# Optimization experiments

Measured on AMD Instinct MI355X. Metric: run time of the kernel, lower is better.

## Reference

```python
import jax, jax.numpy as jnp
import numpy as np

DIM = 1024
HEADS = 16
DIM_HEAD = 64
INNER = HEADS * DIM_HEAD  # 1024
EPS = 1e-5


def setup_inputs() -> dict:
    key = jax.random.key(0)
    ks = jax.random.split(key, 8)
    B, N = 4, 2048
    s = 0.02
    return {
        "query": jax.random.normal(ks[0], (B, N, DIM), jnp.float32),
        "key_": jax.random.normal(ks[1], (B, N, DIM), jnp.float32),
        "value": jax.random.normal(ks[2], (B, N, DIM), jnp.float32),
        "Wq": jax.random.normal(ks[3], (DIM, INNER), jnp.float32) * s,
        "Wk": jax.random.normal(ks[4], (DIM, INNER), jnp.float32) * s,
        "Wv": jax.random.normal(ks[5], (DIM, INNER), jnp.float32) * s,
        "Wo": jax.random.normal(ks[6], (INNER, DIM), jnp.float32) * s,
        "bo": jnp.zeros((DIM,), jnp.float32),
        "gamma": jnp.ones((DIM,), jnp.float32),
        "beta": jnp.zeros((DIM,), jnp.float32),
    }


def reference(query, key_, value, Wq, Wk, Wv, Wo, bo, gamma, beta):
    B, N, _ = query.shape
    scale = DIM_HEAD ** (-0.5)
    # project and split heads: [B, H, N, Dh]
    q = (query @ Wq).reshape(B, N, HEADS, DIM_HEAD).transpose(0, 2, 1, 3)
    k = (key_ @ Wk).reshape(B, N, HEADS, DIM_HEAD).transpose(0, 2, 1, 3)
    v = (value @ Wv).reshape(B, N, HEADS, DIM_HEAD).transpose(0, 2, 1, 3)
    dots = jnp.einsum("bhnd,bhmd->bhnm", q, k) * scale  # [B,H,N,N]
    attn = jax.nn.softmax(dots, axis=-1)
    out = jnp.einsum("bhnm,bhmd->bhnd", attn, v)
    out = out.transpose(0, 2, 1, 3).reshape(B, N, INNER)
    out = out @ Wo + bo  # dropout p=0.0 is identity
    # LayerNorm over last dim
    mu = out.mean(-1, keepdims=True)
    var = ((out - mu) ** 2).mean(-1, keepdims=True)
    normed = (out - mu) * jax.lax.rsqrt(var + EPS) * gamma + beta
    return normed + query
```

## Files before the change

kernel.cpp:

```cpp
#include <hip/hip_runtime.h>
#include <stdint.h>

#define K_DIM 1024
#define B_SZ 4
#define N_SEQ 2048
#define HEADS 16
#define DH 64
#define M_TOT (B_SZ * N_SEQ)

typedef __bf16 bf16x8 __attribute__((ext_vector_type(8)));
typedef __bf16 bf16x4 __attribute__((ext_vector_type(4)));
typedef float f32x4 __attribute__((ext_vector_type(4)));
typedef short s16x4 __attribute__((ext_vector_type(4)));

typedef const uint32_t __attribute__((address_space(1))) gas_u32;
typedef uint32_t __attribute__((address_space(3))) las_u32;

#define CE_SCALE 0.1803368801f

__device__ __forceinline__ uint16_t f2bf(float f) {
  uint32_t u = __float_as_uint(f);
  u += 0x7FFFu + ((u >> 16) & 1u);
  return (uint16_t)(u >> 16);
}

__device__ __forceinline__ void gld_lds16(const uint16_t* g, uint16_t* lds) {
  __builtin_amdgcn_global_load_lds((gas_u32*)g, (las_u32*)lds, 16, 0, 0);
}

#if defined(__has_builtin)
#if __has_builtin(__builtin_amdgcn_mfma_f32_16x16x16bf16_1k)
#define HAVE_MFMA16_BUILTIN 1
#endif
#endif

__device__ __forceinline__ f32x4 mfma16(bf16x4 a, bf16x4 b, f32x4 c) {
#ifdef HAVE_MFMA16_BUILTIN
  return __builtin_amdgcn_mfma_f32_16x16x16bf16_1k(
      __builtin_bit_cast(s16x4, a), __builtin_bit_cast(s16x4, b), c, 0, 0, 0);
#else
  f32x4 d;
  asm("v_mfma_f32_16x16x16_bf16 %0, %1, %2, %3"
      : "=v"(d)
      : "v"(a), "v"(b), "v"(c));
  return d;
#endif
}

__global__ __launch_bounds__(256) void conv_bf16_k(const float* __restrict__ s0,
                                                   const float* __restrict__ s1,
                                                   const float* __restrict__ s2,
                                                   uint16_t* __restrict__ dstbase, int n4) {
  const int z = blockIdx.y;
  const float* src = (z == 0) ? s0 : (z == 1) ? s1 : s2;
  uint16_t* dst = dstbase + (size_t)z * M_TOT * K_DIM;
  int i = blockIdx.x * blockDim.x + threadIdx.x;
  if (i < n4) {
    float4 v = ((const float4*)src)[i];
    ushort4 o;
    o.x = f2bf(v.x); o.y = f2bf(v.y); o.z = f2bf(v.z); o.w = f2bf(v.w);
    ((ushort4*)dst)[i] = o;
  }
}

__global__ __launch_bounds__(256) void transpose_conv(const float* __restrict__ s0,
                                                      const float* __restrict__ s1,
                                                      const float* __restrict__ s2,
                                                      const float* __restrict__ s3,
                                                      uint16_t* __restrict__ dstbase) {
  __shared__ float tile[32][33];
  const int z = blockIdx.z;
  const float* src = (z == 0) ? s0 : (z == 1) ? s1 : (z == 2) ? s2 : s3;
  uint16_t* dst = dstbase + (size_t)z * 1024 * 1024;
  const int tx = threadIdx.x, ty = threadIdx.y;
  const int bx = blockIdx.x * 32, by = blockIdx.y * 32;
#pragma unroll
  for (int i = 0; i < 32; i += 8)
    tile[ty + i][tx] = src[(size_t)(by + ty + i) * 1024 + bx + tx];
  __syncthreads();
#pragma unroll
  for (int i = 0; i < 32; i += 8)
    dst[(size_t)(bx + ty + i) * 1024 + by + tx] = f2bf(tile[tx][ty + i]);
}

template <int MODE>
__global__ __launch_bounds__(256, 2) void gemm_bf16(const uint16_t* __restrict__ A,
                                                    const uint16_t* __restrict__ BT,
                                                    void* __restrict__ Cout,
                                                    const float* __restrict__ bias) {
  __shared__ __align__(16) uint16_t As[128 * 32];
  __shared__ __align__(16) uint16_t Bs[128 * 32];
  const int tid = threadIdx.x;
  const int wave = tid >> 6, lane = tid & 63;
  const int g = lane >> 4, c16 = lane & 15;

  const int bid = blockIdx.x;
  const int xcd = bid & 7;
  const int l = bid >> 3;
  const int z = (MODE == 3) ? (l >> 6) : 0;
  const int r = l & 63;
  const int n0 = (r & 7) * 128;
  const int m0 = (xcd * 8 + (r >> 3)) * 128;

  const int wr = wave >> 1, wc = wave & 1;
  float scale = 1.f;
  if (MODE == 3) {
    A += (size_t)z * M_TOT * K_DIM;
    BT += (size_t)z * 1024 * 1024;
    scale = (z == 0) ? CE_SCALE : 1.f;
  }

  const f32x4 fzero = {0.f, 0.f, 0.f, 0.f};
  f32x4 acc[4][4];
#pragma unroll
  for (int i = 0; i < 4; ++i)
#pragma unroll
    for (int j = 0; j < 4; ++j) acc[i][j] = fzero;

  const int srow = wave * 32 + (lane >> 2);
  const int scol = (lane & 3) * 8;
  const uint16_t* ag0 = A + (size_t)(m0 + srow) * K_DIM + scol;
  const uint16_t* ag1 = A + (size_t)(m0 + srow + 16) * K_DIM + scol;
  const uint16_t* bg0 = BT + (size_t)(n0 + srow) * K_DIM + scol;
  const uint16_t* bg1 = BT + (size_t)(n0 + srow + 16) * K_DIM + scol;
  uint16_t* la0 = &As[(wave * 32) * 32];
  uint16_t* la1 = &As[(wave * 32 + 16) * 32];
  uint16_t* lb0 = &Bs[(wave * 32) * 32];
  uint16_t* lb1 = &Bs[(wave * 32 + 16) * 32];

  for (int kt = 0; kt < K_DIM / 32; ++kt) {
    __syncthreads();
    gld_lds16(ag0 + kt * 32, la0);
    gld_lds16(ag1 + kt * 32, la1);
    gld_lds16(bg0 + kt * 32, lb0);
    gld_lds16(bg1 + kt * 32, lb1);
    __syncthreads();
    bf16x8 avec[4], bvec[4];
#pragma unroll
    for (int i = 0; i < 4; ++i)
      avec[i] = *(const bf16x8*)&As[(wr * 64 + i * 16 + c16) * 32 + g * 8];
#pragma unroll
    for (int j = 0; j < 4; ++j)
      bvec[j] = *(const bf16x8*)&Bs[(wc * 64 + j * 16 + c16) * 32 + g * 8];
#pragma unroll
    for (int i = 0; i < 4; ++i)
#pragma unroll
      for (int j = 0; j < 4; ++j)
        acc[i][j] = __builtin_amdgcn_mfma_f32_16x16x32_bf16(avec[i], bvec[j], acc[i][j], 0, 0, 0);
  }

#pragma unroll
  for (int i = 0; i < 4; ++i) {
#pragma unroll
    for (int j = 0; j < 4; ++j) {
      const int col = n0 + wc * 64 + j * 16 + c16;
      if (MODE == 3 && z == 2) {
        const int h = col >> 6, d = col & 63;
        const int row0 = m0 + wr * 64 + i * 16 + g * 4;
        const int b = row0 >> 11, n = row0 & 2047;
        ushort4 o;
        o.x = f2bf(acc[i][j][0]); o.y = f2bf(acc[i][j][1]);
        o.z = f2bf(acc[i][j][2]); o.w = f2bf(acc[i][j][3]);
        *(ushort4*)&((uint16_t*)Cout)[(size_t)2 * M_TOT * 1024 +
                                      (((size_t)(b * HEADS + h)) * DH + d) * N_SEQ + n] = o;
      } else {
#pragma unroll
        for (int r2 = 0; r2 < 4; ++r2) {
          const int row = m0 + wr * 64 + i * 16 + g * 4 + r2;
          if (MODE == 3) {
            const int b = row >> 11, n = row & 2047;
            const int h = col >> 6, d = col & 63;
            ((uint16_t*)Cout)[(size_t)z * M_TOT * 1024 +
                              (((size_t)(b * HEADS + h)) * N_SEQ + n) * DH + d] =
                f2bf(acc[i][j][r2] * scale);
          } else {
            ((float*)Cout)[(size_t)row * 1024 + col] = acc[i][j][r2] + bias[col];
          }
        }
      }
    }
  }
}

__global__ __launch_bounds__(256, 2) void attention_k(const uint16_t* __restrict__ qm,
                                                      const uint16_t* __restrict__ km,
                                                      const uint16_t* __restrict__ vtm,
                                                      uint16_t* __restrict__ om) {
  __shared__ __align__(16) uint16_t Ks[64 * 64];
  __shared__ __align__(16) uint16_t Vs[64 * 64];
  const int tid = threadIdx.x;
  const int wave = tid >> 6, lane = tid & 63;
  const int g = lane >> 4, c16 = lane & 15;

  const int bid = blockIdx.x;
  const int xcd = bid & 7;
  const int l0 = bid >> 3;
  const int bh = xcd * 8 + (l0 & 7);
  const int qblk = l0 >> 3;
  const int b = bh >> 4, h = bh & 15;
  const int q0 = qblk * 256 + wave * 64;

  const uint16_t* qbase = qm + (size_t)bh * N_SEQ * DH;
  const uint16_t* kbase = km + (size_t)bh * N_SEQ * DH;
  const uint16_t* vbase = vtm + (size_t)bh * DH * N_SEQ;

  bf16x8 qf[4][2];
#pragma unroll
  for (int qc = 0; qc < 4; ++qc) {
    const uint16_t* qp = qbase + (size_t)(q0 + qc * 16 + c16) * DH + g * 8;
    qf[qc][0] = *(const bf16x8*)qp;
    qf[qc][1] = *(const bf16x8*)(qp + 32);
  }

  const f32x4 fz = {0.f, 0.f, 0.f, 0.f};
  f32x4 oacc[4][4];
#pragma unroll
  for (int qc = 0; qc < 4; ++qc)
#pragma unroll
    for (int jt = 0; jt < 4; ++jt) oacc[qc][jt] = fz;
  float l[4] = {0.f, 0.f, 0.f, 0.f};

  const int sw = c16 & 7;

  const int ch = tid & 7;
  const int krow0 = tid >> 3, krow1 = (256 + tid) >> 3;
  const int kdst0 = krow0 * 64 + ((ch ^ (krow0 & 7)) << 3);
  const int kdst1 = krow1 * 64 + ((ch ^ (krow1 & 7)) << 3);

  uint4 kp0, kp1, vp0, vp1;
  kp0 = *(const uint4*)&kbase[(size_t)tid * 8];
  kp1 = *(const uint4*)&kbase[(size_t)(256 + tid) * 8];
  vp0 = *(const uint4*)&vbase[(size_t)krow0 * N_SEQ + ch * 8];
  vp1 = *(const uint4*)&vbase[(size_t)krow1 * N_SEQ + ch * 8];
  *(uint4*)&Ks[kdst0] = kp0;
  *(uint4*)&Ks[kdst1] = kp1;
  *(uint4*)&Vs[kdst0] = vp0;
  *(uint4*)&Vs[kdst1] = vp1;
  __syncthreads();

  for (int t = 0; t < N_SEQ / 64; ++t) {
    if (t < N_SEQ / 64 - 1) {
      const size_t ko = (size_t)(t + 1) * 4096;
      const int vc = (t + 1) * 64;
      kp0 = *(const uint4*)&kbase[ko + (size_t)tid * 8];
      kp1 = *(const uint4*)&kbase[ko + (size_t)(256 + tid) * 8];
      vp0 = *(const uint4*)&vbase[(size_t)krow0 * N_SEQ + vc + ch * 8];
      vp1 = *(const uint4*)&vbase[(size_t)krow1 * N_SEQ + vc + ch * 8];
    }

#pragma unroll
    for (int kt = 0; kt < 4; ++kt) {
      const int krow = kt * 16 + c16;
      bf16x8 kf0 = *(const bf16x8*)&Ks[krow * 64 + ((g ^ sw) << 3)];
      bf16x8 kf1 = *(const bf16x8*)&Ks[krow * 64 + (((4 + g) ^ sw) << 3)];
      bf16x4 pk[4];
#pragma unroll
      for (int qc = 0; qc < 4; ++qc) {
        f32x4 z = fz;
        z = __builtin_amdgcn_mfma_f32_16x16x32_bf16(kf0, qf[qc][0], z, 0, 0, 0);
        z = __builtin_amdgcn_mfma_f32_16x16x32_bf16(kf1, qf[qc][1], z, 0, 0, 0);
        const float p0 = __builtin_amdgcn_exp2f(z[0]);
        const float p1 = __builtin_amdgcn_exp2f(z[1]);
        const float p2 = __builtin_amdgcn_exp2f(z[2]);
        const float p3 = __builtin_amdgcn_exp2f(z[3]);
        l[qc] += (p0 + p1) + (p2 + p3);
        bf16x4 pq;
        pq[0] = (__bf16)p0; pq[1] = (__bf16)p1; pq[2] = (__bf16)p2; pq[3] = (__bf16)p3;
        pk[qc] = pq;
      }
#pragma unroll
      for (int jt = 0; jt < 4; ++jt) {
        bf16x4 vb = *(const bf16x4*)&Vs[(jt * 16 + c16) * 64 +
                                        (((kt * 2 + (g >> 1)) ^ sw) << 3) + (g & 1) * 4];
#pragma unroll
        for (int qc = 0; qc < 4; ++qc) oacc[qc][jt] = mfma16(pk[qc], vb, oacc[qc][jt]);
      }
    }

    if (t < N_SEQ / 64 - 1) {
      __syncthreads();
      *(uint4*)&Ks[kdst0] = kp0;
      *(uint4*)&Ks[kdst1] = kp1;
      *(uint4*)&Vs[kdst0] = vp0;
      *(uint4*)&Vs[kdst1] = vp1;
      __syncthreads();
    }
  }

#pragma unroll
  for (int qc = 0; qc < 4; ++qc) {
    l[qc] += __shfl_xor(l[qc], 16);
    l[qc] += __shfl_xor(l[qc], 32);
  }

#pragma unroll
  for (int qc = 0; qc < 4; ++qc) {
#pragma unroll
    for (int r = 0; r < 4; ++r) {
      const float lr = __shfl(l[qc], g * 4 + r, 16);
      const float inv = 1.f / lr;
      const int row = q0 + qc * 16 + g * 4 + r;
      const size_t base = ((size_t)b * N_SEQ + row) * 1024 + h * 64;
#pragma unroll
      for (int jt = 0; jt < 4; ++jt)
        om[base + jt * 16 + c16] = f2bf(oacc[qc][jt][r] * inv);
    }
  }
}

__global__ __launch_bounds__(256) void ln_res_k(const float* __restrict__ proj,
                                                const float* __restrict__ query,
                                                const float* __restrict__ gamma,
                                                const float* __restrict__ beta,
                                                float* __restrict__ out) {
  const int row = blockIdx.x;
  const int tid = threadIdx.x;
  const size_t base = (size_t)row * 1024 + tid * 4;
  float4 v = *(const float4*)(proj + base);
  float s = v.x + v.y + v.z + v.w;
  float s2 = v.x * v.x + v.y * v.y + v.z * v.z + v.w * v.w;
#pragma unroll
  for (int off = 1; off < 64; off <<= 1) {
    s += __shfl_xor(s, off);
    s2 += __shfl_xor(s2, off);
  }
  __shared__ float red[8];
  const int wave = tid >> 6, lane = tid & 63;
  if (lane == 0) { red[wave] = s; red[4 + wave] = s2; }
  __syncthreads();
  s = red[0] + red[1] + red[2] + red[3];
  s2 = red[4] + red[5] + red[6] + red[7];
  const float mu = s * (1.f / 1024.f);
  const float var = fmaxf(s2 * (1.f / 1024.f) - mu * mu, 0.f);
  const float rstd = rsqrtf(var + 1e-5f);
  float4 gq = *(const float4*)(gamma + tid * 4);
  float4 bq = *(const float4*)(beta + tid * 4);
  float4 qq = *(const float4*)(query + base);
  float4 o;
  o.x = (v.x - mu) * rstd * gq.x + bq.x + qq.x;
  o.y = (v.y - mu) * rstd * gq.y + bq.y + qq.y;
  o.z = (v.z - mu) * rstd * gq.z + bq.z + qq.z;
  o.w = (v.w - mu) * rstd * gq.w + bq.w + qq.w;
  *(float4*)(out + base) = o;
}

extern "C" void kernel_launch(void* const* d_in, const int* in_sizes, int n_in,
                              void* d_out, int out_size, void* d_ws, size_t ws_size,
                              hipStream_t stream) {
  (void)in_sizes; (void)n_in; (void)out_size; (void)ws_size;
  const float* query = (const float*)d_in[0];
  const float* key_ = (const float*)d_in[1];
  const float* value = (const float*)d_in[2];
  const float* Wq = (const float*)d_in[3];
  const float* Wk = (const float*)d_in[4];
  const float* Wv = (const float*)d_in[5];
  const float* Wo = (const float*)d_in[6];
  const float* bo = (const float*)d_in[7];
  const float* gamma = (const float*)d_in[8];
  const float* beta = (const float*)d_in[9];
  float* out = (float*)d_out;

  const size_t NELEM = (size_t)M_TOT * 1024;
  uint16_t* wsp = (uint16_t*)d_ws;
  uint16_t* WqT = wsp;
  uint16_t* WoT = WqT + 3 * 1024 * 1024;
  uint16_t* xq = WqT + 4 * 1024 * 1024;
  uint16_t* qb = xq + 3 * NELEM;
  uint16_t* attnO = xq;
  float* proj = (float*)(xq + NELEM);

  const int n4 = (int)(NELEM / 4);
  conv_bf16_k<<<dim3(8192, 3), 256, 0, stream>>>(query, key_, value, xq, n4);

  transpose_conv<<<dim3(32, 32, 4), dim3(32, 8), 0, stream>>>(Wq, Wk, Wv, Wo, WqT);

  gemm_bf16<3><<<1536, 256, 0, stream>>>(xq, WqT, qb, nullptr);

  attention_k<<<512, 256, 0, stream>>>(qb, qb + NELEM, qb + 2 * NELEM, attnO);

  gemm_bf16<1><<<512, 256, 0, stream>>>(attnO, WoT, proj, bo);

  ln_res_k<<<8192, 256, 0, stream>>>(proj, query, gamma, beta, out);
}
```

Baseline: 351.7 us.

## Split attention KV range across wave pairs and reduce partial outputs in LDS

Each attention block now handles 128 queries instead of 256, with two wave pairs each processing half of the key/value sequence. Their partial outputs and row sums are combined through shared memory at the end. K/V tiles are loaded with direct global-to-LDS loads instead of register staging. The grid doubles to 1024 blocks and launch bounds are raised to 4 blocks per SM, to improve occupancy and parallelism. The cost is an extra LDS reduction, the loss of the register prefetch overlap, and two barriers per tile.

```diff
diff --git a/kernel.cpp b/kernel.cpp
--- a/kernel.cpp
+++ b/kernel.cpp
@@ -182,15 +182,18 @@
   }
 }
 
-__global__ __launch_bounds__(256, 2) void attention_k(const uint16_t* __restrict__ qm,
+__global__ __launch_bounds__(256, 4) void attention_k(const uint16_t* __restrict__ qm,
                                                       const uint16_t* __restrict__ km,
                                                       const uint16_t* __restrict__ vtm,
                                                       uint16_t* __restrict__ om) {
-  __shared__ __align__(16) uint16_t Ks[64 * 64];
-  __shared__ __align__(16) uint16_t Vs[64 * 64];
+  __shared__ __align__(16) char smem[36864];
+  uint16_t* KsB = (uint16_t*)smem;
+  uint16_t* VsB = (uint16_t*)smem + 8192;
+
   const int tid = threadIdx.x;
   const int wave = tid >> 6, lane = tid & 63;
   const int g = lane >> 4, c16 = lane & 15;
+  const int qhalf = wave & 1, khalf = wave >> 1;
 
   const int bid = blockIdx.x;
   const int xcd = bid & 7;
@@ -198,11 +201,14 @@
   const int bh = xcd * 8 + (l0 & 7);
   const int qblk = l0 >> 3;
   const int b = bh >> 4, h = bh & 15;
-  const int q0 = qblk * 256 + wave * 64;
+  const int q0 = qblk * 128 + qhalf * 64;
 
   const uint16_t* qbase = qm + (size_t)bh * N_SEQ * DH;
   const uint16_t* kbase = km + (size_t)bh * N_SEQ * DH;
   const uint16_t* vbase = vtm + (size_t)bh * DH * N_SEQ;
+
+  uint16_t* Ksp = KsB + khalf * 4096;
+  uint16_t* Vsp = VsB + khalf * 4096;
 
   bf16x8 qf[4][2];
 #pragma unroll
@@ -222,88 +228,89 @@
 
   const int sw = c16 & 7;
 
-  const int ch = tid & 7;
-  const int krow0 = tid >> 3, krow1 = (256 + tid) >> 3;
-  const int kdst0 = krow0 * 64 + ((ch ^ (krow0 & 7)) << 3);
-  const int kdst1 = krow1 * 64 + ((ch ^ (krow1 & 7)) << 3);
-
-  uint4 kp0, kp1, vp0, vp1;
-  kp0 = *(const uint4*)&kbase[(size_t)tid * 8];
-  kp1 = *(const uint4*)&kbase[(size_t)(256 + tid) * 8];
-  vp0 = *(const uint4*)&vbase[(size_t)krow0 * N_SEQ + ch * 8];
-  vp1 = *(const uint4*)&vbase[(size_t)krow1 * N_SEQ + ch * 8];
-  *(uint4*)&Ks[kdst0] = kp0;
-  *(uint4*)&Ks[kdst1] = kp1;
-  *(uint4*)&Vs[kdst0] = vp0;
-  *(uint4*)&Vs[kdst1] = vp1;
-  __syncthreads();
-
-  for (int t = 0; t < N_SEQ / 64; ++t) {
-    if (t < N_SEQ / 64 - 1) {
-      const size_t ko = (size_t)(t + 1) * 4096;
-      const int vc = (t + 1) * 64;
-      kp0 = *(const uint4*)&kbase[ko + (size_t)tid * 8];
-      kp1 = *(const uint4*)&kbase[ko + (size_t)(256 + tid) * 8];
-      vp0 = *(const uint4*)&vbase[(size_t)krow0 * N_SEQ + vc + ch * 8];
-      vp1 = *(const uint4*)&vbase[(size_t)krow1 * N_SEQ + vc + ch * 8];
-    }
+  const int rr8 = lane >> 3, cc = lane & 7;
+  const int chp = (cc ^ rr8) << 3;
+
+  for (int tt = 0; tt < 16; ++tt) {
+    const int t = khalf * 16 + tt;
+    __syncthreads();
+#pragma unroll
+    for (int jj = 0; jj < 4; ++jj) {
+      const int j = qhalf * 4 + jj;
+      const int row = j * 8 + rr8;
+      gld_lds16(kbase + (size_t)t * 4096 + row * 64 + chp, Ksp + j * 512);
+      gld_lds16(vbase + (size_t)row * N_SEQ + t * 64 + chp, Vsp + j * 512);
+    }
+    __syncthreads();
 
 #pragma unroll
     for (int kt = 0; kt < 4; ++kt) {
       const int krow = kt * 16 + c16;
-      bf16x8 kf0 = *(const bf16x8*)&Ks[krow * 64 + ((g ^ sw) << 3)];
-      bf16x8 kf1 = *(const bf16x8*)&Ks[krow * 64 + (((4 + g) ^ sw) << 3)];
+      bf16x8 kf0 = *(const bf16x8*)&Ksp[krow * 64 + ((g ^ sw) << 3)];
+      bf16x8 kf1 = *(const bf16x8*)&Ksp[krow * 64 + (((4 + g) ^ sw) << 3)];
       bf16x4 pk[4];
 #pragma unroll
       for (int qc = 0; qc < 4; ++qc) {
         f32x4 z = fz;
         z = __builtin_amdgcn_mfma_f32_16x16x32_bf16(kf0, qf[qc][0], z, 0, 0, 0);
         z = __builtin_amdgcn_mfma_f32_16x16x32_bf16(kf1, qf[qc][1], z, 0, 0, 0);
-        const float p0 = __builtin_amdgcn_exp2f(z[0]);
-        const float p1 = __builtin_amdgcn_exp2f(z[1]);
-        const float p2 = __builtin_amdgcn_exp2f(z[2]);
-        const float p3 = __builtin_amdgcn_exp2f(z[3]);
-        l[qc] += (p0 + p1) + (p2 + p3);
-        bf16x4 pq;
-        pq[0] = (__bf16)p0; pq[1] = (__bf16)p1; pq[2] = (__bf16)p2; pq[3] = (__bf16)p3;
-        pk[qc] = pq;
+        f32x4 pv;
+        pv[0] = __builtin_amdgcn_exp2f(z[0]);
+        pv[1] = __builtin_amdgcn_exp2f(z[1]);
+        pv[2] = __builtin_amdgcn_exp2f(z[2]);
+        pv[3] = __builtin_amdgcn_exp2f(z[3]);
+        l[qc] += (pv[0] + pv[1]) + (pv[2] + pv[3]);
+        pk[qc] = __builtin_convertvector(pv, bf16x4);
       }
 #pragma unroll
       for (int jt = 0; jt < 4; ++jt) {
-        bf16x4 vb = *(const bf16x4*)&Vs[(jt * 16 + c16) * 64 +
-                                        (((kt * 2 + (g >> 1)) ^ sw) << 3) + (g & 1) * 4];
+        bf16x4 vb = *(const bf16x4*)&Vsp[(jt * 16 + c16) * 64 +
+                                         (((kt * 2 + (g >> 1)) ^ sw) << 3) + (g & 1) * 4];
 #pragma unroll
         for (int qc = 0; qc < 4; ++qc) oacc[qc][jt] = mfma16(pk[qc], vb, oacc[qc][jt]);
       }
     }
-
-    if (t < N_SEQ / 64 - 1) {
-      __syncthreads();
-      *(uint4*)&Ks[kdst0] = kp0;
-      *(uint4*)&Ks[kdst1] = kp1;
-      *(uint4*)&Vs[kdst0] = vp0;
-      *(uint4*)&Vs[kdst1] = vp1;
-      __syncthreads();
-    }
-  }
-
-#pragma unroll
-  for (int qc = 0; qc < 4; ++qc) {
-    l[qc] += __shfl_xor(l[qc], 16);
-    l[qc] += __shfl_xor(l[qc], 32);
-  }
-
-#pragma unroll
-  for (int qc = 0; qc < 4; ++qc) {
-#pragma unroll
-    for (int r = 0; r < 4; ++r) {
-      const float lr = __shfl(l[qc], g * 4 + r, 16);
-      const float inv = 1.f / lr;
-      const int row = q0 + qc * 16 + g * 4 + r;
-      const size_t base = ((size_t)b * N_SEQ + row) * 1024 + h * 64;
+  }
+
+  __syncthreads();
+  float* obuf = (float*)smem;
+  float* lbuf = (float*)(smem + 34816);
+  if (khalf == 1) {
+#pragma unroll
+    for (int qc = 0; qc < 4; ++qc) {
 #pragma unroll
       for (int jt = 0; jt < 4; ++jt)
-        om[base + jt * 16 + c16] = f2bf(oacc[qc][jt][r] * inv);
+#pragma unroll
+        for (int rr = 0; rr < 4; ++rr)
+          obuf[qhalf * 4352 + (qc * 16 + g * 4 + rr) * 68 + jt * 16 + c16] = oacc[qc][jt][rr];
+      lbuf[qhalf * 256 + qc * 64 + lane] = l[qc];
+    }
+  }
+  __syncthreads();
+  if (khalf == 0) {
+#pragma unroll
+    for (int qc = 0; qc < 4; ++qc) {
+      l[qc] += lbuf[qhalf * 256 + qc * 64 + lane];
+      l[qc] += __shfl_xor(l[qc], 16);
+      l[qc] += __shfl_xor(l[qc], 32);
+#pragma unroll
+      for (int jt = 0; jt < 4; ++jt)
+#pragma unroll
+        for (int rr = 0; rr < 4; ++rr)
+          oacc[qc][jt][rr] += obuf[qhalf * 4352 + (qc * 16 + g * 4 + rr) * 68 + jt * 16 + c16];
+    }
+#pragma unroll
+    for (int qc = 0; qc < 4; ++qc) {
+#pragma unroll
+      for (int r = 0; r < 4; ++r) {
+        const float lr = __shfl(l[qc], g * 4 + r, 16);
+        const float inv = 1.f / lr;
+        const int row = q0 + qc * 16 + g * 4 + r;
+        const size_t base = ((size_t)b * N_SEQ + row) * 1024 + h * 64;
+#pragma unroll
+        for (int jt = 0; jt < 4; ++jt)
+          om[base + jt * 16 + c16] = f2bf(oacc[qc][jt][r] * inv);
+      }
     }
   }
 }
@@ -376,7 +383,7 @@
 
   gemm_bf16<3><<<1536, 256, 0, stream>>>(xq, WqT, qb, nullptr);
 
-  attention_k<<<512, 256, 0, stream>>>(qb, qb + NELEM, qb + 2 * NELEM, attnO);
+  attention_k<<<1024, 256, 0, stream>>>(qb, qb + NELEM, qb + 2 * NELEM, attnO);
 
   gemm_bf16<1><<<512, 256, 0, stream>>>(attnO, WoT, proj, bo);
 
```

New measurement: 936.0 us. 2.66x slower.

## Fuse fp32-to-bf16 input conversion into QKV GEMM A-tile loading

Applied to the files above, without the earlier changes.

Drops the separate conversion kernel that wrote bf16 copies of query/key/value. The QKV GEMM now reads fp32 activations straight into registers, converts them to bf16 and stores them into LDS, prefetching the next K-slice while the current one computes. The aim is to remove a full read-plus-write pass over three 32MB inputs and one launch. In exchange each GEMM block reads fp32, twice the bytes, and the A tiles are re-read by all 8 column blocks, using register stores instead of direct global-to-LDS loads. The attention exp-to-bf16 packing is also switched to a vector convert.

```diff
diff --git a/kernel.cpp b/kernel.cpp
--- a/kernel.cpp
+++ b/kernel.cpp
@@ -11,6 +11,7 @@
 typedef __bf16 bf16x8 __attribute__((ext_vector_type(8)));
 typedef __bf16 bf16x4 __attribute__((ext_vector_type(4)));
 typedef float f32x4 __attribute__((ext_vector_type(4)));
+typedef float f32x8 __attribute__((ext_vector_type(8)));
 typedef short s16x4 __attribute__((ext_vector_type(4)));
 
 typedef const uint32_t __attribute__((address_space(1))) gas_u32;
@@ -47,22 +48,6 @@
 #endif
 }
 
-__global__ __launch_bounds__(256) void conv_bf16_k(const float* __restrict__ s0,
-                                                   const float* __restrict__ s1,
-                                                   const float* __restrict__ s2,
-                                                   uint16_t* __restrict__ dstbase, int n4) {
-  const int z = blockIdx.y;
-  const float* src = (z == 0) ? s0 : (z == 1) ? s1 : s2;
-  uint16_t* dst = dstbase + (size_t)z * M_TOT * K_DIM;
-  int i = blockIdx.x * blockDim.x + threadIdx.x;
-  if (i < n4) {
-    float4 v = ((const float4*)src)[i];
-    ushort4 o;
-    o.x = f2bf(v.x); o.y = f2bf(v.y); o.z = f2bf(v.z); o.w = f2bf(v.w);
-    ((ushort4*)dst)[i] = o;
-  }
-}
-
 __global__ __launch_bounds__(256) void transpose_conv(const float* __restrict__ s0,
                                                       const float* __restrict__ s1,
                                                       const float* __restrict__ s2,
@@ -83,11 +68,11 @@
     dst[(size_t)(bx + ty + i) * 1024 + by + tx] = f2bf(tile[tx][ty + i]);
 }
 
-template <int MODE>
-__global__ __launch_bounds__(256, 2) void gemm_bf16(const uint16_t* __restrict__ A,
-                                                    const uint16_t* __restrict__ BT,
-                                                    void* __restrict__ Cout,
-                                                    const float* __restrict__ bias) {
+__global__ __launch_bounds__(256, 2) void gemm_qkv(const float* __restrict__ Aq,
+                                                   const float* __restrict__ Ak,
+                                                   const float* __restrict__ Av,
+                                                   const uint16_t* __restrict__ BT,
+                                                   uint16_t* __restrict__ Cout) {
   __shared__ __align__(16) uint16_t As[128 * 32];
   __shared__ __align__(16) uint16_t Bs[128 * 32];
   const int tid = threadIdx.x;
@@ -97,18 +82,118 @@
   const int bid = blockIdx.x;
   const int xcd = bid & 7;
   const int l = bid >> 3;
-  const int z = (MODE == 3) ? (l >> 6) : 0;
+  const int z = l >> 6;
   const int r = l & 63;
   const int n0 = (r & 7) * 128;
   const int m0 = (xcd * 8 + (r >> 3)) * 128;
 
   const int wr = wave >> 1, wc = wave & 1;
-  float scale = 1.f;
-  if (MODE == 3) {
-    A += (size_t)z * M_TOT * K_DIM;
-    BT += (size_t)z * 1024 * 1024;
-    scale = (z == 0) ? CE_SCALE : 1.f;
-  }
+  const float* A = (z == 0) ? Aq : (z == 1) ? Ak : Av;
+  const uint16_t* Bz = BT + (size_t)z * 1024 * 1024;
+  const float scale = (z == 0) ? CE_SCALE : 1.f;
+
+  const f32x4 fzero = {0.f, 0.f, 0.f, 0.f};
+  f32x4 acc[4][4];
+#pragma unroll
+  for (int i = 0; i < 4; ++i)
+#pragma unroll
+    for (int j = 0; j < 4; ++j) acc[i][j] = fzero;
+
+  const int srow = wave * 32 + (lane >> 2);
+  const int scol = (lane & 3) * 8;
+  const float* ag0 = A + (size_t)(m0 + srow) * K_DIM + scol;
+  const float* ag1 = A + (size_t)(m0 + srow + 16) * K_DIM + scol;
+  const uint16_t* bg0 = Bz + (size_t)(n0 + srow) * K_DIM + scol;
+  const uint16_t* bg1 = Bz + (size_t)(n0 + srow + 16) * K_DIM + scol;
+  uint16_t* lb0 = &Bs[(wave * 32) * 32];
+  uint16_t* lb1 = &Bs[(wave * 32 + 16) * 32];
+  uint16_t* la0 = &As[srow * 32 + scol];
+  uint16_t* la1 = &As[(srow + 16) * 32 + scol];
+
+  f32x4 ar0, ar1, ar2, ar3;
+  ar0 = *(const f32x4*)(ag0);
+  ar1 = *(const f32x4*)(ag0 + 4);
+  ar2 = *(const f32x4*)(ag1);
+  ar3 = *(const f32x4*)(ag1 + 4);
+
+  for (int kt = 0; kt < K_DIM / 32; ++kt) {
+    __syncthreads();
+    {
+      f32x8 f0 = __builtin_shufflevector(ar0, ar1, 0, 1, 2, 3, 4, 5, 6, 7);
+      f32x8 f1 = __builtin_shufflevector(ar2, ar3, 0, 1, 2, 3, 4, 5, 6, 7);
+      *(bf16x8*)la0 = __builtin_convertvector(f0, bf16x8);
+      *(bf16x8*)la1 = __builtin_convertvector(f1, bf16x8);
+    }
+    gld_lds16(bg0 + kt * 32, lb0);
+    gld_lds16(bg1 + kt * 32, lb1);
+    __syncthreads();
+
+    if (kt < K_DIM / 32 - 1) {
+      const int ko = (kt + 1) * 32;
+      ar0 = *(const f32x4*)(ag0 + ko);
+      ar1 = *(const f32x4*)(ag0 + ko + 4);
+      ar2 = *(const f32x4*)(ag1 + ko);
+      ar3 = *(const f32x4*)(ag1 + ko + 4);
+    }
+
+    bf16x8 avec[4], bvec[4];
+#pragma unroll
+    for (int i = 0; i < 4; ++i)
+      avec[i] = *(const bf16x8*)&As[(wr * 64 + i * 16 + c16) * 32 + g * 8];
+#pragma unroll
+    for (int j = 0; j < 4; ++j)
+      bvec[j] = *(const bf16x8*)&Bs[(wc * 64 + j * 16 + c16) * 32 + g * 8];
+#pragma unroll
+    for (int i = 0; i < 4; ++i)
+#pragma unroll
+      for (int j = 0; j < 4; ++j)
+        acc[i][j] = __builtin_amdgcn_mfma_f32_16x16x32_bf16(avec[i], bvec[j], acc[i][j], 0, 0, 0);
+  }
+
+#pragma unroll
+  for (int i = 0; i < 4; ++i) {
+#pragma unroll
+    for (int j = 0; j < 4; ++j) {
+      const int col = n0 + wc * 64 + j * 16 + c16;
+      if (z == 2) {
+        const int h = col >> 6, d = col & 63;
+        const int row0 = m0 + wr * 64 + i * 16 + g * 4;
+        const int b = row0 >> 11, n = row0 & 2047;
+        ushort4 o;
+        o.x = f2bf(acc[i][j][0]); o.y = f2bf(acc[i][j][1]);
+        o.z = f2bf(acc[i][j][2]); o.w = f2bf(acc[i][j][3]);
+        *(ushort4*)&Cout[(size_t)2 * M_TOT * 1024 +
+                         (((size_t)(b * HEADS + h)) * DH + d) * N_SEQ + n] = o;
+      } else {
+#pragma unroll
+        for (int r2 = 0; r2 < 4; ++r2) {
+          const int row = m0 + wr * 64 + i * 16 + g * 4 + r2;
+          const int b = row >> 11, n = row & 2047;
+          const int h = col >> 6, d = col & 63;
+          Cout[(size_t)z * M_TOT * 1024 + (((size_t)(b * HEADS + h)) * N_SEQ + n) * DH + d] =
+              f2bf(acc[i][j][r2] * scale);
+        }
+      }
+    }
+  }
+}
+
+__global__ __launch_bounds__(256, 2) void gemm_out(const uint16_t* __restrict__ A,
+                                                   const uint16_t* __restrict__ BT,
+                                                   float* __restrict__ Cout,
+                                                   const float* __restrict__ bias) {
+  __shared__ __align__(16) uint16_t As[128 * 32];
+  __shared__ __align__(16) uint16_t Bs[128 * 32];
+  const int tid = threadIdx.x;
+  const int wave = tid >> 6, lane = tid & 63;
+  const int g = lane >> 4, c16 = lane & 15;
+
+  const int bid = blockIdx.x;
+  const int xcd = bid & 7;
+  const int l = bid >> 3;
+  const int n0 = (l & 7) * 128;
+  const int m0 = (xcd * 8 + (l >> 3)) * 128;
+  const int wr = wave >> 1, wc = wave & 1;
 
   const f32x4 fzero = {0.f, 0.f, 0.f, 0.f};
   f32x4 acc[4][4];
@@ -154,29 +239,10 @@
 #pragma unroll
     for (int j = 0; j < 4; ++j) {
       const int col = n0 + wc * 64 + j * 16 + c16;
-      if (MODE == 3 && z == 2) {
-        const int h = col >> 6, d = col & 63;
-        const int row0 = m0 + wr * 64 + i * 16 + g * 4;
-        const int b = row0 >> 11, n = row0 & 2047;
-        ushort4 o;
-        o.x = f2bf(acc[i][j][0]); o.y = f2bf(acc[i][j][1]);
-        o.z = f2bf(acc[i][j][2]); o.w = f2bf(acc[i][j][3]);
-        *(ushort4*)&((uint16_t*)Cout)[(size_t)2 * M_TOT * 1024 +
-                                      (((size_t)(b * HEADS + h)) * DH + d) * N_SEQ + n] = o;
-      } else {
-#pragma unroll
-        for (int r2 = 0; r2 < 4; ++r2) {
-          const int row = m0 + wr * 64 + i * 16 + g * 4 + r2;
-          if (MODE == 3) {
-            const int b = row >> 11, n = row & 2047;
-            const int h = col >> 6, d = col & 63;
-            ((uint16_t*)Cout)[(size_t)z * M_TOT * 1024 +
-                              (((size_t)(b * HEADS + h)) * N_SEQ + n) * DH + d] =
-                f2bf(acc[i][j][r2] * scale);
-          } else {
-            ((float*)Cout)[(size_t)row * 1024 + col] = acc[i][j][r2] + bias[col];
-          }
-        }
+#pragma unroll
+      for (int r2 = 0; r2 < 4; ++r2) {
+        const int row = m0 + wr * 64 + i * 16 + g * 4 + r2;
+        Cout[(size_t)row * 1024 + col] = acc[i][j][r2] + bias[col];
       }
     }
   }
@@ -259,14 +325,13 @@
         f32x4 z = fz;
         z = __builtin_amdgcn_mfma_f32_16x16x32_bf16(kf0, qf[qc][0], z, 0, 0, 0);
         z = __builtin_amdgcn_mfma_f32_16x16x32_bf16(kf1, qf[qc][1], z, 0, 0, 0);
-        const float p0 = __builtin_amdgcn_exp2f(z[0]);
-        const float p1 = __builtin_amdgcn_exp2f(z[1]);
-        const float p2 = __builtin_amdgcn_exp2f(z[2]);
-        const float p3 = __builtin_amdgcn_exp2f(z[3]);
-        l[qc] += (p0 + p1) + (p2 + p3);
-        bf16x4 pq;
-        pq[0] = (__bf16)p0; pq[1] = (__bf16)p1; pq[2] = (__bf16)p2; pq[3] = (__bf16)p3;
-        pk[qc] = pq;
+        f32x4 pv;
+        pv[0] = __builtin_amdgcn_exp2f(z[0]);
+        pv[1] = __builtin_amdgcn_exp2f(z[1]);
+        pv[2] = __builtin_amdgcn_exp2f(z[2]);
+        pv[3] = __builtin_amdgcn_exp2f(z[3]);
+        l[qc] += (pv[0] + pv[1]) + (pv[2] + pv[3]);
+        pk[qc] = __builtin_convertvector(pv, bf16x4);
       }
 #pragma unroll
       for (int jt = 0; jt < 4; ++jt) {
@@ -364,21 +429,17 @@
   uint16_t* wsp = (uint16_t*)d_ws;
   uint16_t* WqT = wsp;
   uint16_t* WoT = WqT + 3 * 1024 * 1024;
-  uint16_t* xq = WqT + 4 * 1024 * 1024;
-  uint16_t* qb = xq + 3 * NELEM;
-  uint16_t* attnO = xq;
-  float* proj = (float*)(xq + NELEM);
-
-  const int n4 = (int)(NELEM / 4);
-  conv_bf16_k<<<dim3(8192, 3), 256, 0, stream>>>(query, key_, value, xq, n4);
+  uint16_t* qb = wsp + 4 * 1024 * 1024;
+  uint16_t* attnO = qb + 3 * NELEM;
+  float* proj = (float*)(attnO + NELEM);
 
   transpose_conv<<<dim3(32, 32, 4), dim3(32, 8), 0, stream>>>(Wq, Wk, Wv, Wo, WqT);
 
-  gemm_bf16<3><<<1536, 256, 0, stream>>>(xq, WqT, qb, nullptr);
+  gemm_qkv<<<1536, 256, 0, stream>>>(query, key_, value, WqT, qb);
 
   attention_k<<<512, 256, 0, stream>>>(qb, qb + NELEM, qb + 2 * NELEM, attnO);
 
-  gemm_bf16<1><<<512, 256, 0, stream>>>(attnO, WoT, proj, bo);
+  gemm_out<<<512, 256, 0, stream>>>(attnO, WoT, proj, bo);
 
   ln_res_k<<<8192, 256, 0, stream>>>(proj, query, gamma, beta, out);
 }
```

After: 367.4 us. 1.04x slower.
